# Optimization experiments

Measured on AMD Instinct MI355X. Metric: run time of the kernel, lower is better.

## Reference

```python
import jax, jax.numpy as jnp
import numpy as np

B, L, V, E, H = 64, 32, 32000, 512, 1024


def setup_inputs() -> dict:
    key = jax.random.key(0)
    ks = jax.random.split(key, 12)
    s = 0.02
    return {
        "x": jax.random.randint(ks[0], (B, 4 * L), 0, V, dtype=jnp.int32),
        "IsTrain": 1,
        "embedding": jax.random.normal(ks[1], (V, E), jnp.float32) * s,
        "W_csm": jax.random.normal(ks[2], (E, H), jnp.float32) * s,
        "Wx1": jax.random.normal(ks[3], (H, H), jnp.float32) * s,
        "Wh1": jax.random.normal(ks[4], (H, H), jnp.float32) * s,
        "Wx2": jax.random.normal(ks[5], (H, H), jnp.float32) * s,
        "Wh2": jax.random.normal(ks[6], (H, H), jnp.float32) * s,
        "U": jax.random.normal(ks[7], (L, H, H), jnp.float32) * s,
        "Ww": jax.random.normal(ks[8], (V, H), jnp.float32) * s,
        "Wc": jax.random.normal(ks[9], (H, H), jnp.float32) * s,
        "Wfc": jax.random.normal(ks[10], (H, V), jnp.float32) * s,
    }


def _forward(x, embedding, W_csm, Wx1, Wh1, Wx2, Wh2, U, Ww, Wc, Wfc):
    # x: [B, 4L] int token ids (train mode: 4 sentences)
    emb = embedding[x]                                   # [B, 4L, E]

    # CSM: sentence -> vector [B, H] (mean-pool + projection + tanh)
    segs = emb[:, : 3 * L].reshape(x.shape[0], 3, L, E)  # first 3 sentences
    sent = jnp.tanh(jnp.einsum("bse,eh->bsh", segs.mean(axis=2), W_csm))  # [B,3,H]

    # RCM: 2-layer tanh RNN over sentence vectors; hidden after t sentences
    # equals RCM run on the length-t prefix (prefix property of an RNN).
    def step(carry, s_t):
        h1, h2 = carry
        h1 = jnp.tanh(s_t @ Wx1 + h1 @ Wh1)
        h2 = jnp.tanh(h1 @ Wx2 + h2 @ Wh2)
        return (h1, h2), h2

    h0 = jnp.zeros((x.shape[0], H), emb.dtype)
    _, hs = jax.lax.scan(step, (h0, h0), sent.transpose(1, 0, 2))  # [3,B,H]

    # Per-position context vectors: context_k = tanh(h_k @ U_m) for m in [0,L)
    contexts = jnp.tanh(jnp.einsum("sbh,mhk->sbmk", hs, U))        # [3,B,L,H]

    # RGM at step i (i>=1 within each section): prev hidden is always re-zeroed
    # in the original loop, so cur = tanh(onehot(w) @ Ww + ctx @ Wc); the one-hot
    # matmul is expressed as a gather (identical math).
    # Section k, local step i in [1,L): word index = x[:, (k+1)*L + i - 1]
    idx = jnp.stack([x[:, (k + 1) * L : (k + 2) * L - 1] for k in range(3)])  # [3,B,L-1]
    cur = jnp.tanh(Ww[idx] + jnp.einsum("sblh,hk->sblk", contexts[:, :, 1:], Wc))
    y_sec = jnp.einsum("sblh,hv->sblv", cur, Wfc)                  # [3,B,L-1,V]

    # Step 0 of each section: one-hot of the first target word (constant wrt params)
    firsts = x[:, jnp.array([L, 2 * L, 3 * L])].T                   # [3,B]
    first_oh = jax.nn.one_hot(firsts, V, dtype=y_sec.dtype)         # [3,B,V]

    y = jnp.concatenate([first_oh[:, :, None, :], y_sec], axis=2)   # [3,B,L,V]
    return y.transpose(1, 0, 2, 3).reshape(x.shape[0], 3 * L, V)


def reference(x, IsTrain, embedding, W_csm, Wx1, Wh1, Wx2, Wh2, U, Ww, Wc, Wfc):
    # IsTrain must be truthy: this reference implements the training branch.
    return _forward(x, embedding, W_csm, Wx1, Wh1, Wx2, Wh2, U, Ww, Wc, Wfc)
```

## Files before the change

kernel.cpp:

```cpp
#include <hip/hip_runtime.h>
#include <math.h>

typedef __bf16 bf16x8 __attribute__((ext_vector_type(8)));
typedef float f32x4 __attribute__((ext_vector_type(4)));
typedef unsigned short u16;

#define DI __device__ __forceinline__

DI u16 f2bf(float f) {
  union { float f; unsigned u; } v; v.f = f;
  unsigned r = v.u + 0x7FFFu + ((v.u >> 16) & 1u);
  return (u16)(r >> 16);
}

DI void gload_lds16(const u16* g, u16* l) {
  __builtin_amdgcn_global_load_lds(
      (const __attribute__((address_space(1))) unsigned int*)g,
      (__attribute__((address_space(3))) unsigned int*)l, 16, 0, 0);
}

__global__ __launch_bounds__(256) void onehot_k(const int* __restrict__ x,
                                                float* __restrict__ out) {
  int bid = blockIdx.x;
  int bs = bid >> 3, chunk = bid & 7;
  int s = bs >> 6, b = bs & 63;
  long base = ((long)b * 96 + s * 32) * 32000;
  float4* o4 = (float4*)(out + base) + chunk * 1000;
  float4 z; z.x = z.y = z.z = z.w = 0.f;
  for (int i = threadIdx.x; i < 1000; i += 256) o4[i] = z;
  __syncthreads();
  if (threadIdx.x == 0) {
    int tok = x[b * 128 + (s + 1) * 32];
    if (tok / 4000 == chunk) out[base + tok] = 1.0f;
  }
}

__global__ __launch_bounds__(256) void meanpool_k(const int* __restrict__ x,
    const float* __restrict__ emb, u16* __restrict__ sentM) {
  int bs = blockIdx.x; int s = bs >> 6, b = bs & 63;
  int t = threadIdx.x;
  float a0 = 0.f, a1 = 0.f;
  for (int lt = 0; lt < 32; ++lt) {
    int tok = x[b * 128 + s * 32 + lt];
    const float* e = emb + (long)tok * 512;
    a0 += e[t]; a1 += e[t + 256];
  }
  sentM[(long)bs * 512 + t] = f2bf(a0 * (1.f / 32.f));
  sentM[(long)bs * 512 + t + 256] = f2bf(a1 * (1.f / 32.f));
}

__global__ __launch_bounds__(256) void transpose_cvt(
    const float* __restrict__ in, u16* __restrict__ out, int R, int C,
    int ostride) {
  in += (long)blockIdx.z * R * C;
  out += (long)blockIdx.z * (long)C * ostride;
  __shared__ float tile[32][33];
  int c0 = blockIdx.x * 32, r0 = blockIdx.y * 32;
  int tx = threadIdx.x & 31, ty = threadIdx.x >> 5;
#pragma unroll
  for (int i = 0; i < 4; ++i)
    tile[ty + 8 * i][tx] = in[(long)(r0 + ty + 8 * i) * C + c0 + tx];
  __syncthreads();
#pragma unroll
  for (int i = 0; i < 4; ++i)
    out[(long)(c0 + ty + 8 * i) * ostride + r0 + tx] = f2bf(tile[tx][ty + 8 * i]);
}

__global__ __launch_bounds__(256) void gemm_small(
    const u16* __restrict__ A0, const u16* __restrict__ A1,
    const u16* __restrict__ Bt, u16* __restrict__ outp,
    int M, int K, int kSplit, int Astride, int Bstride) {
  int mt = blockIdx.x, ntb = blockIdx.y;
  __shared__ __align__(16) u16 As[2048];
  __shared__ __align__(16) u16 Bs[4096];
  const int t = threadIdx.x;
  const int w = t >> 6, l = t & 63, lr = l & 15, lg = l >> 4;
  int ar = mt * 64 + (t & 63); if (ar >= M) ar = M - 1;
  const u16* pB = Bt + (long)(ntb * 128 + (t & 127)) * Bstride + (t >> 7) * 8;
  f32x4 acc[4][2] = {};
  for (int k0 = 0; k0 < K; k0 += 32) {
    __syncthreads();
    const u16* srcA = (k0 < kSplit)
        ? A0 + (long)ar * Astride + k0 + w * 8
        : A1 + (long)ar * 1024 + (k0 - kSplit) + w * 8;
    gload_lds16(srcA, As + w * 512);
    gload_lds16(pB + k0, Bs + w * 512);
    gload_lds16(pB + k0 + 16, Bs + 2048 + w * 512);
    __syncthreads();
    bf16x8 a[4], b[2];
#pragma unroll
    for (int mf = 0; mf < 4; ++mf)
      a[mf] = *(const bf16x8*)(As + (lg * 64 + mf * 16 + lr) * 8);
#pragma unroll
    for (int nf = 0; nf < 2; ++nf)
      b[nf] = *(const bf16x8*)(Bs + (lg * 128 + w * 32 + nf * 16 + lr) * 8);
#pragma unroll
    for (int mf = 0; mf < 4; ++mf)
#pragma unroll
      for (int nf = 0; nf < 2; ++nf)
        acc[mf][nf] = __builtin_amdgcn_mfma_f32_16x16x32_bf16(a[mf], b[nf], acc[mf][nf], 0, 0, 0);
  }
#pragma unroll
  for (int mf = 0; mf < 4; ++mf)
#pragma unroll
    for (int j = 0; j < 4; ++j) {
      int r = mt * 64 + mf * 16 + lg * 4 + j;
      if (r < M) {
        u16* o = outp + (long)r * 1024 + ntb * 128 + w * 32;
#pragma unroll
        for (int nf = 0; nf < 2; ++nf)
          o[nf * 16 + lr] = f2bf(tanhf(acc[mf][nf][j]));
      }
    }
}

template <int MODE>
__global__ __launch_bounds__(256) void gemm_bf16(
    const u16* __restrict__ A, const u16* __restrict__ Bt,
    const float* __restrict__ Ww, const int* __restrict__ xtok,
    void* __restrict__ outp, int M) {
  int mt = blockIdx.x, nt = blockIdx.y, mz = blockIdx.z;
  if constexpr (MODE == 0) Bt += (long)mz << 20;

  __shared__ __align__(16) u16 As[128 * 32];
  __shared__ __align__(16) u16 Bs[128 * 32];

  const int t = threadIdx.x;
  const int w = t >> 6, l = t & 63;
  const int lr = l & 15, lg = l >> 4;
  const int wr = w >> 1, wc = w & 1;

  int ar0 = mt * 128 + (t >> 2);
  int ar1 = ar0 + 64;
  if (ar0 >= M) ar0 = 0;
  if (ar1 >= M) ar1 = 0;
  long arow0, arow1;
  if constexpr (MODE == 1) {
    arow0 = (long)(ar0 / 31) * 32 + (ar0 % 31) + 1;
    arow1 = (long)(ar1 / 31) * 32 + (ar1 % 31) + 1;
  } else {
    arow0 = ar0; arow1 = ar1;
  }

  const u16* ga0 = A + arow0 * 1024 + (t & 3) * 8;
  const u16* ga1 = A + arow1 * 1024 + (t & 3) * 8;
  const u16* gb0 = Bt + ((long)nt * 128 + (t >> 2)) * 1024 + (t & 3) * 8;
  const u16* gb1 = gb0 + 64 * 1024;

  u16* dA0 = As + w * 512; u16* dA1 = As + 2048 + w * 512;
  u16* dB0 = Bs + w * 512; u16* dB1 = Bs + 2048 + w * 512;

  f32x4 acc[4][4] = {};

  for (int kt = 0; kt < 32; ++kt) {
    __syncthreads();
    gload_lds16(ga0, dA0); gload_lds16(ga1, dA1);
    gload_lds16(gb0, dB0); gload_lds16(gb1, dB1);
    ga0 += 32; ga1 += 32; gb0 += 32; gb1 += 32;
    __syncthreads();
    bf16x8 a[4], b[4];
#pragma unroll
    for (int m = 0; m < 4; ++m)
      a[m] = *(const bf16x8*)&As[(wr * 64 + m * 16 + lr) * 32 + lg * 8];
#pragma unroll
    for (int n = 0; n < 4; ++n)
      b[n] = *(const bf16x8*)&Bs[(wc * 64 + n * 16 + lr) * 32 + lg * 8];
#pragma unroll
    for (int m = 0; m < 4; ++m)
#pragma unroll
      for (int n = 0; n < 4; ++n)
        acc[m][n] = __builtin_amdgcn_mfma_f32_16x16x32_bf16(a[m], b[n], acc[m][n], 0, 0, 0);
  }

#pragma unroll
  for (int m = 0; m < 4; ++m) {
#pragma unroll
    for (int j = 0; j < 4; ++j) {
      int r = mt * 128 + wr * 64 + m * 16 + lg * 4 + j;
      if (r >= M) continue;
      if constexpr (MODE == 0) {
        u16* oc = (u16*)outp;
#pragma unroll
        for (int n = 0; n < 4; ++n) {
          int col = nt * 128 + wc * 64 + n * 16 + lr;
          oc[((long)r * 32 + mz) * 1024 + col] = f2bf(tanhf(acc[m][n][j]));
        }
      } else {
        int sb = r / 31, l1 = r % 31;
        int s = sb >> 6, b = sb & 63;
        int widx = xtok[b * 128 + (s + 1) * 32 + l1];
        const float* wwr = Ww + (long)widx * 1024;
        u16* oc = (u16*)outp;
#pragma unroll
        for (int n = 0; n < 4; ++n) {
          int col = nt * 128 + wc * 64 + n * 16 + lr;
          oc[(long)r * 1024 + col] = f2bf(tanhf(acc[m][n][j] + wwr[col]));
        }
      }
    }
  }
}

#define NOSTAGE ((void)0)
#define VM4 asm volatile("s_waitcnt vmcnt(4)" ::: "memory")
#define VM0 asm volatile("s_waitcnt vmcnt(0)" ::: "memory")

#define STAGE_A(H, KT) do {                                                \
    const u16* _s = ((H) ? pA1 : pA0) + (KT) * 64;                         \
    u16* _d = lds + ((KT) & 1) * 16384 + (H) * 8192 + w * 512;             \
    gload_lds16(_s, _d); gload_lds16(_s + 32, _d + 4096);                  \
  } while (0)
#define STAGE_B(H, KT) do {                                                \
    const u16* _s = ((H) ? pB1 : pB0) + (KT) * 64;                         \
    u16* _d = lds + 32768 + ((KT) & 1) * 16384 + (H) * 8192 + w * 512;     \
    gload_lds16(_s, _d); gload_lds16(_s + 32, _d + 4096);                  \
  } while (0)

#define PHASE(ABASE, MH, NH, RA, RB, STAGESTMT, WAITSTMT) do {             \
    if (RA) {                                                              \
      _Pragma("unroll") for (int ks = 0; ks < 2; ++ks)                     \
      _Pragma("unroll") for (int mf = 0; mf < 4; ++mf)                     \
        a[mf][ks] = *(const bf16x8*)(lds + (ABASE) + (MH) * 8192 + laneA + \
                                     ks * 4096 + mf * 128);                \
    }                                                                      \
    if (RB) {                                                              \
      _Pragma("unroll") for (int ks = 0; ks < 2; ++ks)                     \
      _Pragma("unroll") for (int nf = 0; nf < 2; ++nf)                     \
        b[NH][nf][ks] = *(const bf16x8*)(lds + 32768 + (ABASE) +           \
                                         (NH) * 8192 + laneB +             \
                                         ks * 4096 + nf * 128);            \
    }                                                                      \
    STAGESTMT;                                                             \
    __builtin_amdgcn_s_barrier();                                          \
    asm volatile("s_waitcnt lgkmcnt(0)" ::: "memory");                     \
    __builtin_amdgcn_sched_barrier(0);                                     \
    __builtin_amdgcn_s_setprio(1);                                         \
    _Pragma("unroll") for (int ks = 0; ks < 2; ++ks)                       \
    _Pragma("unroll") for (int mf = 0; mf < 4; ++mf)                       \
    _Pragma("unroll") for (int nf = 0; nf < 2; ++nf)                       \
      acc[(MH) * 4 + mf][(NH) * 2 + nf] =                                  \
          __builtin_amdgcn_mfma_f32_16x16x32_bf16(                         \
              a[mf][ks], b[NH][nf][ks],                                    \
              acc[(MH) * 4 + mf][(NH) * 2 + nf], 0, 0, 0);                 \
    __builtin_amdgcn_s_setprio(0);                                         \
    WAITSTMT;                                                              \
    __builtin_amdgcn_s_barrier();                                          \
  } while (0)

__global__ __launch_bounds__(512, 2) void gemm_big(
    const u16* __restrict__ A, const u16* __restrict__ Bt,
    float* __restrict__ out) {
  int bid = blockIdx.x;
  int wg = (bid & 7) * 375 + (bid >> 3);
  int mt = wg % 24, nt = wg / 24;

  __shared__ __align__(16) u16 lds[65536];

  const int t = threadIdx.x;
  const int w = t >> 6, l = t & 63;
  const int lr = l & 15, lg = l >> 4;
  const int wm = w >> 2, wn = w & 3;
  const int laneA = (lg * 128 + wm * 64 + lr) * 8;
  const int laneB = (lg * 128 + wn * 32 + lr) * 8;

  int arow0 = mt * 256 + (t & 127);
  int arow1 = arow0 + 128;
  if (arow0 > 5951) arow0 = 5951;
  if (arow1 > 5951) arow1 = 5951;
  const u16* pA0 = A + (long)arow0 * 1024 + (t >> 7) * 8;
  const u16* pA1 = A + (long)arow1 * 1024 + (t >> 7) * 8;
  const u16* pB0 = Bt + ((long)nt * 256 + (t & 127)) * 1024 + (t >> 7) * 8;
  const u16* pB1 = pB0 + 128 * 1024;

  f32x4 acc[8][4] = {};
  bf16x8 a[4][2], b[2][2][2];

  STAGE_A(0, 0); STAGE_B(0, 0); STAGE_B(1, 0); STAGE_A(1, 0);
  STAGE_A(0, 1); STAGE_B(0, 1);
  VM4;
  __builtin_amdgcn_s_barrier();

  for (int g = 0; g < 14; g += 2) {
    PHASE(0,     0, 0, 1, 1, STAGE_B(1, g + 1), NOSTAGE);
    PHASE(0,     0, 1, 0, 1, STAGE_A(1, g + 1), NOSTAGE);
    PHASE(0,     1, 0, 1, 0, STAGE_A(0, g + 2), NOSTAGE);
    PHASE(0,     1, 1, 0, 0, STAGE_B(0, g + 2), VM4);
    PHASE(16384, 0, 0, 1, 1, STAGE_B(1, g + 2), NOSTAGE);
    PHASE(16384, 0, 1, 0, 1, STAGE_A(1, g + 2), NOSTAGE);
    PHASE(16384, 1, 0, 1, 0, STAGE_A(0, g + 3), NOSTAGE);
    PHASE(16384, 1, 1, 0, 0, STAGE_B(0, g + 3), VM4);
  }
  PHASE(0,     0, 0, 1, 1, STAGE_B(1, 15), NOSTAGE);
  PHASE(0,     0, 1, 0, 1, STAGE_A(1, 15), NOSTAGE);
  PHASE(0,     1, 0, 1, 0, NOSTAGE, NOSTAGE);
  PHASE(0,     1, 1, 0, 0, NOSTAGE, VM0);
  PHASE(16384, 0, 0, 1, 1, NOSTAGE, NOSTAGE);
  PHASE(16384, 0, 1, 0, 1, NOSTAGE, NOSTAGE);
  PHASE(16384, 1, 0, 1, 0, NOSTAGE, NOSTAGE);
  PHASE(16384, 1, 1, 0, 0, NOSTAGE, NOSTAGE);

#pragma unroll
  for (int mh = 0; mh < 2; ++mh)
#pragma unroll
    for (int mf = 0; mf < 4; ++mf)
#pragma unroll
      for (int j = 0; j < 4; ++j) {
        int r = mt * 256 + mh * 128 + wm * 64 + mf * 16 + lg * 4 + j;
        if (r < 5952) {
          int s = r / 1984, rem = r % 1984;
          int bb = rem / 31, l1 = rem % 31;
          float* o = out + ((long)bb * 96 + s * 32 + l1 + 1) * 32000 +
                     nt * 256 + wn * 32;
#pragma unroll
          for (int nh = 0; nh < 2; ++nh)
#pragma unroll
            for (int nf = 0; nf < 2; ++nf)
              o[nh * 128 + nf * 16 + lr] = acc[mh * 4 + mf][nh * 2 + nf][j];
        }
      }
}

extern "C" void kernel_launch(void* const* d_in, const int* in_sizes, int n_in,
                              void* d_out, int out_size, void* d_ws, size_t ws_size,
                              hipStream_t stream) {
  const int*   x    = (const int*)d_in[0];
  const float* emb  = (const float*)d_in[2];
  const float* Wcsm = (const float*)d_in[3];
  const float* Wx1  = (const float*)d_in[4];
  const float* Wh1  = (const float*)d_in[5];
  const float* Wx2  = (const float*)d_in[6];
  const float* Wh2  = (const float*)d_in[7];
  const float* U    = (const float*)d_in[8];
  const float* Ww   = (const float*)d_in[9];
  const float* Wc   = (const float*)d_in[10];
  const float* Wfc  = (const float*)d_in[11];
  float* out = (float*)d_out;

  char* ws = (char*)d_ws;
  u16* sentM = (u16*)(ws + 0);
  u16* sentH = (u16*)(ws + 196608);
  u16* h1a   = (u16*)(ws + 589824);
  u16* h1b   = (u16*)(ws + 720896);
  u16* hsb   = (u16*)(ws + 851968);
  u16* ctx   = (u16*)(ws + 1245184);
  u16* WcsmT = (u16*)(ws + 1245184);
  u16* WxhT1 = (u16*)(ws + 2293760);
  u16* WxhT2 = (u16*)(ws + 6488064);
  u16* cur   = (u16*)(ws + 13828096);
  u16* WcT   = (u16*)(ws + 26017792);
  u16* BIG   = (u16*)(ws + 28114944);

  onehot_k<<<1536, 256, 0, stream>>>(x, out);

  transpose_cvt<<<dim3(32, 16, 1), 256, 0, stream>>>(Wcsm, WcsmT, 512, 1024, 512);
  transpose_cvt<<<dim3(32, 32, 1), 256, 0, stream>>>(Wx1, WxhT1, 1024, 1024, 2048);
  transpose_cvt<<<dim3(32, 32, 1), 256, 0, stream>>>(Wh1, WxhT1 + 1024, 1024, 1024, 2048);
  transpose_cvt<<<dim3(32, 32, 1), 256, 0, stream>>>(Wx2, WxhT2, 1024, 1024, 2048);
  transpose_cvt<<<dim3(32, 32, 1), 256, 0, stream>>>(Wh2, WxhT2 + 1024, 1024, 1024, 2048);
  transpose_cvt<<<dim3(32, 32, 1), 256, 0, stream>>>(Wc, WcT, 1024, 1024, 1024);

  meanpool_k<<<192, 256, 0, stream>>>(x, emb, sentM);
  gemm_small<<<dim3(3, 8), 256, 0, stream>>>(sentM, sentM, WcsmT, sentH, 192, 512, 512, 512, 512);

  gemm_small<<<dim3(1, 8), 256, 0, stream>>>(sentH,          h1a, WxhT1, h1a,           64, 1024, 1024, 1024, 2048);
  gemm_small<<<dim3(1, 8), 256, 0, stream>>>(h1a,            h1a, WxhT2, hsb,           64, 1024, 1024, 1024, 2048);
  gemm_small<<<dim3(1, 8), 256, 0, stream>>>(sentH + 65536,  h1a, WxhT1, h1b,           64, 2048, 1024, 1024, 2048);
  gemm_small<<<dim3(1, 8), 256, 0, stream>>>(h1b,            hsb, WxhT2, hsb + 65536,   64, 2048, 1024, 1024, 2048);
  gemm_small<<<dim3(1, 8), 256, 0, stream>>>(sentH + 131072, h1b, WxhT1, h1a,           64, 2048, 1024, 1024, 2048);
  gemm_small<<<dim3(1, 8), 256, 0, stream>>>(h1a, hsb + 65536, WxhT2, hsb + 131072,     64, 2048, 1024, 1024, 2048);

  transpose_cvt<<<dim3(32, 32, 32), 256, 0, stream>>>(U, BIG, 1024, 1024, 1024);
  gemm_bf16<0><<<dim3(2, 8, 32), 256, 0, stream>>>(hsb, BIG, nullptr, nullptr, (void*)ctx, 192);

  gemm_bf16<1><<<dim3(47, 8, 1), 256, 0, stream>>>(ctx, WcT, Ww, x, (void*)cur, 5952);

  transpose_cvt<<<dim3(1000, 32, 1), 256, 0, stream>>>(Wfc, BIG, 1024, 32000, 1024);
  gemm_big<<<3000, 512, 0, stream>>>(cur, BIG, out);
}
```

Baseline: 999.5 us.

## Vectorize transposes, batch weight transposes, pipeline gemm_small, and coalesce gemm_big stores

```diff
diff --git a/kernel.cpp b/kernel.cpp
--- a/kernel.cpp
+++ b/kernel.cpp
@@ -4,6 +4,7 @@
 typedef __bf16 bf16x8 __attribute__((ext_vector_type(8)));
 typedef float f32x4 __attribute__((ext_vector_type(4)));
 typedef unsigned short u16;
+typedef u16 u16x8 __attribute__((ext_vector_type(8)));
 
 #define DI __device__ __forceinline__
 
@@ -49,21 +50,40 @@
   sentM[(long)bs * 512 + t + 256] = f2bf(a1 * (1.f / 32.f));
 }
 
-__global__ __launch_bounds__(256) void transpose_cvt(
+DI void transpose64_body(const float* __restrict__ in, u16* __restrict__ out,
+                         int C, int ostride) {
+  __shared__ float tile[32 * 65];
+  int c0 = blockIdx.x * 32, r0 = blockIdx.y * 64;
+  int t = threadIdx.x;
+  int cc = t & 31, rr0 = t >> 5;
+#pragma unroll
+  for (int i = 0; i < 8; ++i) {
+    int rr = rr0 + 8 * i;
+    tile[cc * 65 + (rr ^ ((cc & 7) << 3))] = in[(long)(r0 + rr) * C + c0 + cc];
+  }
+  __syncthreads();
+  int cj = t >> 3, rj = t & 7;
+  u16x8 v;
+#pragma unroll
+  for (int k = 0; k < 8; ++k)
+    v[k] = f2bf(tile[cj * 65 + ((rj * 8 + k) ^ ((cj & 7) << 3))]);
+  *(u16x8*)(out + (long)(c0 + cj) * ostride + r0 + rj * 8) = v;
+}
+
+__global__ __launch_bounds__(256) void transpose64(
     const float* __restrict__ in, u16* __restrict__ out, int R, int C,
     int ostride) {
-  in += (long)blockIdx.z * R * C;
+  in += (long)blockIdx.z * (long)R * C;
   out += (long)blockIdx.z * (long)C * ostride;
-  __shared__ float tile[32][33];
-  int c0 = blockIdx.x * 32, r0 = blockIdx.y * 32;
-  int tx = threadIdx.x & 31, ty = threadIdx.x >> 5;
-#pragma unroll
-  for (int i = 0; i < 4; ++i)
-    tile[ty + 8 * i][tx] = in[(long)(r0 + ty + 8 * i) * C + c0 + tx];
-  __syncthreads();
-#pragma unroll
-  for (int i = 0; i < 4; ++i)
-    out[(long)(c0 + ty + 8 * i) * ostride + r0 + tx] = f2bf(tile[tx][ty + 8 * i]);
+  transpose64_body(in, out, C, ostride);
+}
+
+struct TJob { const float* in; u16* out; int R; int ostride; };
+struct TJobs { TJob j[6]; };
+__global__ __launch_bounds__(256) void transpose64_multi(TJobs jobs) {
+  TJob jb = jobs.j[blockIdx.z];
+  if ((int)(blockIdx.y * 64) >= jb.R) return;
+  transpose64_body(jb.in, jb.out, 1024, jb.ostride);
 }
 
 __global__ __launch_bounds__(256) void gemm_small(
@@ -71,34 +91,53 @@
     const u16* __restrict__ Bt, u16* __restrict__ outp,
     int M, int K, int kSplit, int Astride, int Bstride) {
   int mt = blockIdx.x, ntb = blockIdx.y;
-  __shared__ __align__(16) u16 As[2048];
-  __shared__ __align__(16) u16 Bs[4096];
+  __shared__ __align__(16) u16 As[3][2048];
+  __shared__ __align__(16) u16 Bs[3][4096];
   const int t = threadIdx.x;
   const int w = t >> 6, l = t & 63, lr = l & 15, lg = l >> 4;
   int ar = mt * 64 + (t & 63); if (ar >= M) ar = M - 1;
   const u16* pB = Bt + (long)(ntb * 128 + (t & 127)) * Bstride + (t >> 7) * 8;
-  f32x4 acc[4][2] = {};
-  for (int k0 = 0; k0 < K; k0 += 32) {
-    __syncthreads();
+  const int ntk = K >> 5;
+
+  auto STG = [&](int buf, int kt) {
+    int k0 = kt << 5;
     const u16* srcA = (k0 < kSplit)
         ? A0 + (long)ar * Astride + k0 + w * 8
         : A1 + (long)ar * 1024 + (k0 - kSplit) + w * 8;
-    gload_lds16(srcA, As + w * 512);
-    gload_lds16(pB + k0, Bs + w * 512);
-    gload_lds16(pB + k0 + 16, Bs + 2048 + w * 512);
-    __syncthreads();
+    gload_lds16(srcA, &As[buf][w * 512]);
+    gload_lds16(pB + k0, &Bs[buf][w * 512]);
+    gload_lds16(pB + k0 + 16, &Bs[buf][2048 + w * 512]);
+  };
+  STG(0, 0);
+  if (ntk > 1) STG(1, 1);
+
+  f32x4 acc[4][2] = {};
+  for (int kt = 0; kt < ntk; ++kt) {
+    int cb = kt % 3;
+    if (kt + 2 < ntk) {
+      STG((kt + 2) % 3, kt + 2);
+      asm volatile("s_waitcnt vmcnt(6)" ::: "memory");
+    } else if (kt + 1 < ntk) {
+      asm volatile("s_waitcnt vmcnt(3)" ::: "memory");
+    } else {
+      asm volatile("s_waitcnt vmcnt(0)" ::: "memory");
+    }
+    __builtin_amdgcn_s_barrier();
+    __builtin_amdgcn_sched_barrier(0);
     bf16x8 a[4], b[2];
 #pragma unroll
     for (int mf = 0; mf < 4; ++mf)
-      a[mf] = *(const bf16x8*)(As + (lg * 64 + mf * 16 + lr) * 8);
+      a[mf] = *(const bf16x8*)(&As[cb][(lg * 64 + mf * 16 + lr) * 8]);
 #pragma unroll
     for (int nf = 0; nf < 2; ++nf)
-      b[nf] = *(const bf16x8*)(Bs + (lg * 128 + w * 32 + nf * 16 + lr) * 8);
+      b[nf] = *(const bf16x8*)(&Bs[cb][(lg * 128 + w * 32 + nf * 16 + lr) * 8]);
 #pragma unroll
     for (int mf = 0; mf < 4; ++mf)
 #pragma unroll
       for (int nf = 0; nf < 2; ++nf)
         acc[mf][nf] = __builtin_amdgcn_mfma_f32_16x16x32_bf16(a[mf], b[nf], acc[mf][nf], 0, 0, 0);
+    __builtin_amdgcn_s_barrier();
+    __builtin_amdgcn_sched_barrier(0);
   }
 #pragma unroll
   for (int mf = 0; mf < 4; ++mf)
@@ -251,8 +290,9 @@
     const u16* __restrict__ A, const u16* __restrict__ Bt,
     float* __restrict__ out) {
   int bid = blockIdx.x;
-  int wg = (bid & 7) * 375 + (bid >> 3);
-  int mt = wg % 24, nt = wg / 24;
+  int xcd = bid & 7, idx = bid >> 3;
+  int nt = idx / 3;
+  int mt = xcd * 3 + idx % 3;
 
   __shared__ __align__(16) u16 lds[65536];
 
@@ -299,25 +339,36 @@
   PHASE(16384, 1, 0, 1, 0, NOSTAGE, NOSTAGE);
   PHASE(16384, 1, 1, 0, 0, NOSTAGE, NOSTAGE);
 
+  float* T = (float*)lds + w * 2112;
 #pragma unroll
   for (int mh = 0; mh < 2; ++mh)
 #pragma unroll
-    for (int mf = 0; mf < 4; ++mf)
-#pragma unroll
-      for (int j = 0; j < 4; ++j) {
-        int r = mt * 256 + mh * 128 + wm * 64 + mf * 16 + lg * 4 + j;
+    for (int nh = 0; nh < 2; ++nh) {
+#pragma unroll
+      for (int mf = 0; mf < 4; ++mf)
+#pragma unroll
+        for (int j = 0; j < 4; ++j)
+#pragma unroll
+          for (int nf = 0; nf < 2; ++nf)
+            T[(mf * 16 + lg * 4 + j) * 33 + nf * 16 + lr] =
+                acc[mh * 4 + mf][nh * 2 + nf][j];
+#pragma unroll
+      for (int i = 0; i < 8; ++i) {
+        int row = (l >> 3) + 8 * i;
+        int c4 = (l & 7) * 4;
+        f32x4 v;
+        v[0] = T[row * 33 + c4];     v[1] = T[row * 33 + c4 + 1];
+        v[2] = T[row * 33 + c4 + 2]; v[3] = T[row * 33 + c4 + 3];
+        int r = mt * 256 + mh * 128 + wm * 64 + row;
         if (r < 5952) {
           int s = r / 1984, rem = r % 1984;
           int bb = rem / 31, l1 = rem % 31;
           float* o = out + ((long)bb * 96 + s * 32 + l1 + 1) * 32000 +
-                     nt * 256 + wn * 32;
-#pragma unroll
-          for (int nh = 0; nh < 2; ++nh)
-#pragma unroll
-            for (int nf = 0; nf < 2; ++nf)
-              o[nh * 128 + nf * 16 + lr] = acc[mh * 4 + mf][nh * 2 + nf][j];
+                     nt * 256 + nh * 128 + wn * 32 + c4;
+          __builtin_nontemporal_store(v, (f32x4*)o);
         }
       }
+    }
 }
 
 extern "C" void kernel_launch(void* const* d_in, const int* in_sizes, int n_in,
@@ -352,12 +403,14 @@
 
   onehot_k<<<1536, 256, 0, stream>>>(x, out);
 
-  transpose_cvt<<<dim3(32, 16, 1), 256, 0, stream>>>(Wcsm, WcsmT, 512, 1024, 512);
-  transpose_cvt<<<dim3(32, 32, 1), 256, 0, stream>>>(Wx1, WxhT1, 1024, 1024, 2048);
-  transpose_cvt<<<dim3(32, 32, 1), 256, 0, stream>>>(Wh1, WxhT1 + 1024, 1024, 1024, 2048);
-  transpose_cvt<<<dim3(32, 32, 1), 256, 0, stream>>>(Wx2, WxhT2, 1024, 1024, 2048);
-  transpose_cvt<<<dim3(32, 32, 1), 256, 0, stream>>>(Wh2, WxhT2 + 1024, 1024, 1024, 2048);
-  transpose_cvt<<<dim3(32, 32, 1), 256, 0, stream>>>(Wc, WcT, 1024, 1024, 1024);
+  TJobs jobs;
+  jobs.j[0] = {Wx1,  WxhT1,        1024, 2048};
+  jobs.j[1] = {Wh1,  WxhT1 + 1024, 1024, 2048};
+  jobs.j[2] = {Wx2,  WxhT2,        1024, 2048};
+  jobs.j[3] = {Wh2,  WxhT2 + 1024, 1024, 2048};
+  jobs.j[4] = {Wc,   WcT,          1024, 1024};
+  jobs.j[5] = {Wcsm, WcsmT,         512,  512};
+  transpose64_multi<<<dim3(32, 16, 6), 256, 0, stream>>>(jobs);
 
   meanpool_k<<<192, 256, 0, stream>>>(x, emb, sentM);
   gemm_small<<<dim3(3, 8), 256, 0, stream>>>(sentM, sentM, WcsmT, sentH, 192, 512, 512, 512, 512);
@@ -369,11 +422,11 @@
   gemm_small<<<dim3(1, 8), 256, 0, stream>>>(sentH + 131072, h1b, WxhT1, h1a,           64, 2048, 1024, 1024, 2048);
   gemm_small<<<dim3(1, 8), 256, 0, stream>>>(h1a, hsb + 65536, WxhT2, hsb + 131072,     64, 2048, 1024, 1024, 2048);
 
-  transpose_cvt<<<dim3(32, 32, 32), 256, 0, stream>>>(U, BIG, 1024, 1024, 1024);
+  transpose64<<<dim3(32, 16, 32), 256, 0, stream>>>(U, BIG, 1024, 1024, 1024);
   gemm_bf16<0><<<dim3(2, 8, 32), 256, 0, stream>>>(hsb, BIG, nullptr, nullptr, (void*)ctx, 192);
 
   gemm_bf16<1><<<dim3(47, 8, 1), 256, 0, stream>>>(ctx, WcT, Ww, x, (void*)cur, 5952);
 
-  transpose_cvt<<<dim3(1000, 32, 1), 256, 0, stream>>>(Wfc, BIG, 1024, 32000, 1024);
+  transpose64<<<dim3(1000, 16, 1), 256, 0, stream>>>(Wfc, BIG, 1024, 32000, 1024);
   gemm_big<<<3000, 512, 0, stream>>>(cur, BIG, out);
 }
```

After: 922.2 us. 1.08x faster.
